# Optimization experiments

Hardware: AMD Instinct MI355X
Metric: run time of the kernel (lower is better)

## Reference

```python
import jax, jax.numpy as jnp
import numpy as np

B, D, C, T = 2048, 512, 128, 151  # batch, hidden, vocab(NUM_CHAR), TEXT_MAX_LEN


def setup_inputs() -> dict:
    key = jax.random.key(0)
    ks = jax.random.split(key, 8)
    s = 1.0 / np.sqrt(D)
    u = lambda k, shape: jax.random.uniform(k, shape, jnp.float32, -s, s)
    return {
        "feat": jax.random.normal(ks[0], (B, D), jnp.float32),  # resnet pooler_output
        "W_ih": u(ks[1], (3 * D, D)),   # GRU input weights (r,z,n stacked, torch layout)
        "W_hh": u(ks[2], (3 * D, D)),   # GRU hidden weights
        "b_ih": u(ks[3], (3 * D,)),
        "b_hh": u(ks[4], (3 * D,)),
        "W_proj": u(ks[5], (C, D)),     # Linear(512, NUM_CHAR)
        "b_proj": u(ks[6], (C,)),
        "embed": jax.random.normal(ks[7], (C, D), jnp.float32),  # Embedding(NUM_CHAR, 512)
    }


def reference(feat, W_ih, W_hh, b_ih, b_hh, W_proj, b_proj, embed):
    def step(carry, _):
        h, x = carry  # [B,D] each
        gi = x @ W_ih.T + b_ih   # [B,3D]
        gh = h @ W_hh.T + b_hh   # [B,3D]
        i_r, i_z, i_n = jnp.split(gi, 3, axis=1)
        h_r, h_z, h_n = jnp.split(gh, 3, axis=1)
        r = jax.nn.sigmoid(i_r + h_r)
        z = jax.nn.sigmoid(i_z + h_z)
        n = jnp.tanh(i_n + r * h_n)
        h_new = (1.0 - z) * n + z * h
        logits = h_new @ W_proj.T + b_proj          # [B,C]
        probs = jax.nn.softmax(logits, axis=1)
        tok = jnp.argmax(probs, axis=1)             # [B]
        x_new = embed[tok]                          # greedy feedback
        return (h_new, x_new), (logits, tok)

    h0 = feat                                        # hidden init = pooled feature
    x0 = jnp.zeros((feat.shape[0], D), feat.dtype)   # zero start token input
    _, (logits_seq, toks_seq) = jax.lax.scan(step, (h0, x0), None, length=T)
    logits = jnp.transpose(logits_seq, (1, 2, 0))    # [B, NUM_CHAR, T]
    tokens = toks_seq.T                              # [B, T]
    return logits, tokens
```

## Files before the change

kernel.cpp:

```cpp
#include <hip/hip_runtime.h>
#include <math.h>

#define BB 2048
#define DD 512
#define CC 128
#define TT 151
#define G3 1536

typedef __bf16 bf16x8 __attribute__((ext_vector_type(8)));
typedef float f32x4 __attribute__((ext_vector_type(4)));


__global__ void k_transpose_wih(const float* __restrict__ Wih, float* __restrict__ WihT) {
    int idx = blockIdx.x * 256 + threadIdx.x;
    if (idx < G3 * DD) {
        int j = idx / DD, k = idx - j * DD;
        WihT[k * G3 + j] = Wih[idx];
    }
}

__global__ void k_pack_wp_frag(const float* __restrict__ Wproj, __bf16* __restrict__ out) {
    int idx = blockIdx.x * 256 + threadIdx.x;
    if (idx >= 131072) return;
    int j = idx & 7;
    int lane = (idx >> 3) & 63;
    int part = (idx >> 9) & 1;
    int kt = (idx >> 10) & 15;
    int w = idx >> 14;
    int c = w * 16 + (lane & 15);
    int k = kt * 32 + (lane >> 4) * 8 + j;
    float v = Wproj[c * DD + k];
    __bf16 hi = (__bf16)v;
    out[idx] = part ? (__bf16)(v - (float)hi) : hi;
}

__global__ void k_pack_whh_frag(const float* __restrict__ Whh, __bf16* __restrict__ out) {
    int idx = blockIdx.x * 256 + threadIdx.x;
    if (idx >= 786432) return;
    int j8 = idx & 7;
    int lane = (idx >> 3) & 63;
    int rest = idx >> 9;
    int tile = rest % 12;
    int kt = (rest / 12) % 16;
    int w = rest / (12 * 16);
    int g = tile >> 2, tl = tile & 3;
    int colc = lane & 15, quad = lane >> 4;
    int jcol = g * 512 + w * 64 + tl * 16 + colc;
    int k = kt * 32 + quad * 8 + j8;
    float v = Whh[jcol * DD + k];
    __bf16 hi = (__bf16)v;
    __bf16 lo = (__bf16)(v - (float)hi);
    size_t base = ((((size_t)w * 16 + kt) * 12 + tile) * 2) * 512 + lane * 8 + j8;
    out[base] = hi;
    out[base + 512] = lo;
}

__global__ void k_build_E(const float* __restrict__ embed, const float* __restrict__ WihT,
                          const float* __restrict__ b_ih, const float* __restrict__ b_hh,
                          float* __restrict__ E) {
    __shared__ float emb[16][DD];
    const int t = threadIdx.x;
    const int j = blockIdx.x * 256 + t;
    const int c0 = blockIdx.y * 16;
    for (int i = 0; i < 16; i++) {
        int c = c0 + i;
        for (int k = t; k < DD; k += 256)
            emb[i][k] = (c < CC) ? embed[c * DD + k] : 0.0f;
    }
    __syncthreads();
    float acc[16];
#pragma unroll
    for (int i = 0; i < 16; i++) acc[i] = 0.0f;
    for (int k = 0; k < DD; k++) {
        float wv = WihT[k * G3 + j];
#pragma unroll
        for (int i = 0; i < 16; i++) acc[i] = fmaf(emb[i][k], wv, acc[i]);
    }
    float bj = b_ih[j] + (j < 1024 ? b_hh[j] : 0.0f);
    for (int i = 0; i < 16; i++) {
        int c = c0 + i;
        if (c <= CC) E[(size_t)c * G3 + j] = acc[i] + bj;
    }
}


__device__ __forceinline__ float fast_sigmoid(float x) {
    return __builtin_amdgcn_rcpf(1.0f + __expf(-x));
}
__device__ __forceinline__ float fast_tanh(float x) {
    x = fminf(10.0f, fmaxf(-10.0f, x));
    float e = __expf(2.0f * x);
    return (e - 1.0f) * __builtin_amdgcn_rcpf(e + 1.0f);
}

__global__ __launch_bounds__(512, 2) void k_gru(
    const float* __restrict__ feat, const __bf16* __restrict__ Whf,
    const __bf16* __restrict__ Wpf, const float* __restrict__ b_proj,
    const float* __restrict__ b_hh, const float* __restrict__ Ep,
    float* __restrict__ out) {
    __shared__ __align__(16) __bf16 h_hi[16][520];
    __shared__ __align__(16) __bf16 h_lo[16][520];
    __shared__ float lgbuf[16][CC][9];
    __shared__ int tok_s[16];

    float* out_logits = out;
    float* out_tok = out + (size_t)BB * CC * TT;

    const int t = threadIdx.x;
    const int w = t >> 6;
    const int lane = t & 63;
    const int row0 = blockIdx.x * 16;
    const int col = lane & 15;
    const int quad = lane >> 4;
    const int bq = quad * 4;

    float ho[4][4];
#pragma unroll
    for (int tile = 0; tile < 4; tile++) {
        const int d = w * 64 + tile * 16 + col;
#pragma unroll
        for (int rg = 0; rg < 4; rg++) {
            const int b = bq + rg;
            float v = feat[(size_t)(row0 + b) * DD + d];
            ho[tile][rg] = v;
            __bf16 hi = (__bf16)v;
            h_hi[b][d] = hi;
            h_lo[b][d] = (__bf16)(v - (float)hi);
        }
    }
    if (t < 16) tok_s[t] = CC;

    const float bp = b_proj[w * 16 + col];
    float bhn_t[4];
#pragma unroll
    for (int tile = 0; tile < 4; tile++)
        bhn_t[tile] = b_hh[1024 + w * 64 + tile * 16 + col];

    const __bf16* wseq = Whf + (size_t)w * 196608;
    const __bf16* wpseq = Wpf + (size_t)w * 16384;
    __syncthreads();

    for (int step = 0; step < TT; step++) {
        const int sl = step & 7;

        f32x4 acc[12];
#pragma unroll
        for (int i = 0; i < 12; i++) acc[i] = (f32x4)(0.0f);
        for (int kt = 0; kt < 16; kt++) {
            bf16x8 ahi = *(const bf16x8*)&h_hi[col][kt * 32 + quad * 8];
            bf16x8 alo = *(const bf16x8*)&h_lo[col][kt * 32 + quad * 8];
            const __bf16* wk = wseq + kt * 12288;
#pragma unroll
            for (int tile = 0; tile < 12; tile++) {
                bf16x8 bhi = *(const bf16x8*)(wk + tile * 1024 + lane * 8);
                bf16x8 blo = *(const bf16x8*)(wk + tile * 1024 + 512 + lane * 8);
                acc[tile] = __builtin_amdgcn_mfma_f32_16x16x32_bf16(ahi, bhi, acc[tile], 0, 0, 0);
                acc[tile] = __builtin_amdgcn_mfma_f32_16x16x32_bf16(alo, bhi, acc[tile], 0, 0, 0);
                acc[tile] = __builtin_amdgcn_mfma_f32_16x16x32_bf16(ahi, blo, acc[tile], 0, 0, 0);
            }
        }
        __syncthreads();

        {
            int tk[4];
#pragma unroll
            for (int rg = 0; rg < 4; rg++) tk[rg] = tok_s[bq + rg];
#pragma unroll
            for (int tile = 0; tile < 4; tile++) {
                const int d = w * 64 + tile * 16 + col;
#pragma unroll
                for (int rg = 0; rg < 4; rg++) {
                    const int b = bq + rg;
                    const float* Er = Ep + (size_t)tk[rg] * G3 + d;
                    float rr = fast_sigmoid(acc[tile][rg] + Er[0]);
                    float zz = fast_sigmoid(acc[4 + tile][rg] + Er[512]);
                    float nn = fast_tanh(Er[1024] + rr * (acc[8 + tile][rg] + bhn_t[tile]));
                    float hv = (1.0f - zz) * nn + zz * ho[tile][rg];
                    ho[tile][rg] = hv;
                    __bf16 hi = (__bf16)hv;
                    h_hi[b][d] = hi;
                    h_lo[b][d] = (__bf16)(hv - (float)hi);
                }
            }
        }
        __syncthreads();

        {
            f32x4 accp = (f32x4)(0.0f);
            for (int kt = 0; kt < 16; kt++) {
                bf16x8 ahi = *(const bf16x8*)&h_hi[col][kt * 32 + quad * 8];
                bf16x8 alo = *(const bf16x8*)&h_lo[col][kt * 32 + quad * 8];
                const __bf16* pk = wpseq + kt * 1024;
                bf16x8 bhi = *(const bf16x8*)(pk + lane * 8);
                bf16x8 blo = *(const bf16x8*)(pk + 512 + lane * 8);
                accp = __builtin_amdgcn_mfma_f32_16x16x32_bf16(ahi, bhi, accp, 0, 0, 0);
                accp = __builtin_amdgcn_mfma_f32_16x16x32_bf16(alo, bhi, accp, 0, 0, 0);
                accp = __builtin_amdgcn_mfma_f32_16x16x32_bf16(ahi, blo, accp, 0, 0, 0);
            }
#pragma unroll
            for (int rg = 0; rg < 4; rg++)
                lgbuf[bq + rg][w * 16 + col][sl] = accp[rg] + bp;
        }
        __syncthreads();

        {
#pragma unroll
            for (int pass = 0; pass < 2; pass++) {
                const int r = w * 2 + pass;
                float v0 = lgbuf[r][lane][sl];
                float v1 = lgbuf[r][lane + 64][sl];
                float bv; int bi;
                if (v0 >= v1) { bv = v0; bi = lane; } else { bv = v1; bi = lane + 64; }
#pragma unroll
                for (int off = 32; off > 0; off >>= 1) {
                    float ov = __shfl_down(bv, off, 64);
                    int oi = __shfl_down(bi, off, 64);
                    if (ov > bv || (ov == bv && oi < bi)) { bv = ov; bi = oi; }
                }
                if (lane == 0) {
                    tok_s[r] = bi;
                    __builtin_nontemporal_store((float)bi, &out_tok[(size_t)(row0 + r) * TT + step]);
                }
            }
        }
        __syncthreads();

        if ((step & 7) == 7 || step == TT - 1) {
            const int t0 = step & ~7;
            const int cnt = step - t0 + 1;
#pragma unroll
            for (int p = 0; p < 4; p++) {
                const int pair = t + p * 512;
                const int b = pair >> 7, c = pair & (CC - 1);
                float* dst = out_logits + ((size_t)(row0 + b) * CC + c) * TT + t0;
                const float* src = &lgbuf[b][c][0];
                for (int s = 0; s < cnt; s++) __builtin_nontemporal_store(src[s], &dst[s]);
            }
        }
    }
}


extern "C" void kernel_launch(void* const* d_in, const int* in_sizes, int n_in,
                              void* d_out, int out_size, void* d_ws, size_t ws_size,
                              hipStream_t stream) {
    const float* feat   = (const float*)d_in[0];
    const float* W_ih   = (const float*)d_in[1];
    const float* W_hh   = (const float*)d_in[2];
    const float* b_ih   = (const float*)d_in[3];
    const float* b_hh   = (const float*)d_in[4];
    const float* W_proj = (const float*)d_in[5];
    const float* b_proj = (const float*)d_in[6];
    const float* embed  = (const float*)d_in[7];
    float* out = (float*)d_out;

    float* ws = (float*)d_ws;
    float*  WihT = ws;
    float*  E    = ws + 786432;
    __bf16* Wpf  = (__bf16*)(ws + 984576);
    __bf16* Whf  = (__bf16*)(ws + 1050112);

    hipLaunchKernelGGL(k_transpose_wih, dim3(3072), dim3(256), 0, stream, W_ih, WihT);
    hipLaunchKernelGGL(k_pack_wp_frag, dim3(512), dim3(256), 0, stream, W_proj, Wpf);
    hipLaunchKernelGGL(k_pack_whh_frag, dim3(3072), dim3(256), 0, stream, W_hh, Whf);
    hipLaunchKernelGGL(k_build_E, dim3(6, 9), dim3(256), 0, stream, embed, WihT, b_ih, b_hh, E);
    hipLaunchKernelGGL(k_gru, dim3(128), dim3(512), 0, stream,
                       feat, Whf, Wpf, b_proj, b_hh, E, out);
}
```

Before: 5.868 ms.

## Split each batch tile's hidden dimension across two cooperating blocks with flag sync

Each group of 16 batch rows is now handled by two workgroups (256 blocks instead of 128). Each one computes half of the hidden units and half of the projection K-range. Every step, the two partners exchange their hidden halves and partial logits through global memory, using release/acquire flags and a spin-wait. The intent is to use all CUs on the chip for the latency-bound sequential recurrence. The cost is a cross-block handshake and global round-trip each step, and a deadlock risk if the partner blocks are not co-resident.

Measured after the change: 20.76 ms. 3.54x slower.

```diff
diff --git a/kernel.cpp b/kernel.cpp
--- a/kernel.cpp
+++ b/kernel.cpp
@@ -17,21 +17,6 @@
         int j = idx / DD, k = idx - j * DD;
         WihT[k * G3 + j] = Wih[idx];
     }
-}
-
-__global__ void k_pack_wp_frag(const float* __restrict__ Wproj, __bf16* __restrict__ out) {
-    int idx = blockIdx.x * 256 + threadIdx.x;
-    if (idx >= 131072) return;
-    int j = idx & 7;
-    int lane = (idx >> 3) & 63;
-    int part = (idx >> 9) & 1;
-    int kt = (idx >> 10) & 15;
-    int w = idx >> 14;
-    int c = w * 16 + (lane & 15);
-    int k = kt * 32 + (lane >> 4) * 8 + j;
-    float v = Wproj[c * DD + k];
-    __bf16 hi = (__bf16)v;
-    out[idx] = part ? (__bf16)(v - (float)hi) : hi;
 }
 
 __global__ void k_pack_whh_frag(const float* __restrict__ Whh, __bf16* __restrict__ out) {
@@ -40,17 +25,36 @@
     int j8 = idx & 7;
     int lane = (idx >> 3) & 63;
     int rest = idx >> 9;
-    int tile = rest % 12;
-    int kt = (rest / 12) % 16;
-    int w = rest / (12 * 16);
-    int g = tile >> 2, tl = tile & 3;
-    int colc = lane & 15, quad = lane >> 4;
-    int jcol = g * 512 + w * 64 + tl * 16 + colc;
-    int k = kt * 32 + quad * 8 + j8;
+    int tile = rest % 6;
+    int kt = (rest / 6) % 16;
+    int w = (rest / 96) % 8;
+    int s = rest / 768;
+    int g = tile >> 1, tl = tile & 1;
+    int jcol = g * 512 + s * 256 + w * 32 + tl * 16 + (lane & 15);
+    int k = kt * 32 + (lane >> 4) * 8 + j8;
     float v = Whh[jcol * DD + k];
     __bf16 hi = (__bf16)v;
     __bf16 lo = (__bf16)(v - (float)hi);
-    size_t base = ((((size_t)w * 16 + kt) * 12 + tile) * 2) * 512 + lane * 8 + j8;
+    size_t base = (size_t)((((s * 8 + w) * 16 + kt) * 6 + tile) * 2) * 512 + lane * 8 + j8;
+    out[base] = hi;
+    out[base + 512] = lo;
+}
+
+__global__ void k_pack_wp_frag(const float* __restrict__ Wproj, __bf16* __restrict__ out) {
+    int idx = blockIdx.x * 256 + threadIdx.x;
+    if (idx >= 65536) return;
+    int j = idx & 7;
+    int lane = (idx >> 3) & 63;
+    int rest = idx >> 9;
+    int kt = rest % 8;
+    int w = (rest / 8) % 8;
+    int s = rest / 64;
+    int c = w * 16 + (lane & 15);
+    int k = s * 256 + kt * 32 + (lane >> 4) * 8 + j;
+    float v = Wproj[c * DD + k];
+    __bf16 hi = (__bf16)v;
+    __bf16 lo = (__bf16)(v - (float)hi);
+    size_t base = (size_t)(((s * 8 + w) * 8 + kt) * 2) * 512 + lane * 8 + j;
     out[base] = hi;
     out[base + 512] = lo;
 }
@@ -97,10 +101,13 @@
     const float* __restrict__ feat, const __bf16* __restrict__ Whf,
     const __bf16* __restrict__ Wpf, const float* __restrict__ b_proj,
     const float* __restrict__ b_hh, const float* __restrict__ Ep,
+    unsigned int* xh, float* xl, int* flags,
     float* __restrict__ out) {
     __shared__ __align__(16) __bf16 h_hi[16][520];
     __shared__ __align__(16) __bf16 h_lo[16][520];
-    __shared__ float lgbuf[16][CC][9];
+    __shared__ float plg[16][CC];
+    __shared__ float lgbuf[16][64][10];
+    __shared__ float bpj[CC];
     __shared__ int tok_s[16];
 
     float* out_logits = out;
@@ -109,49 +116,60 @@
     const int t = threadIdx.x;
     const int w = t >> 6;
     const int lane = t & 63;
-    const int row0 = blockIdx.x * 16;
     const int col = lane & 15;
     const int quad = lane >> 4;
     const int bq = quad * 4;
 
-    float ho[4][4];
-#pragma unroll
-    for (int tile = 0; tile < 4; tile++) {
-        const int d = w * 64 + tile * 16 + col;
-#pragma unroll
-        for (int rg = 0; rg < 4; rg++) {
-            const int b = bq + rg;
-            float v = feat[(size_t)(row0 + b) * DD + d];
-            ho[tile][rg] = v;
-            __bf16 hi = (__bf16)v;
-            h_hi[b][d] = hi;
-            h_lo[b][d] = (__bf16)(v - (float)hi);
-        }
-    }
+    const int bid = blockIdx.x;
+    const int grp = bid & 7;
+    const int s = grp >> 2;
+    const int pair = (bid >> 3) * 4 + (grp & 3);
+    const int row0 = pair * 16;
+    const int fl_self = pair * 2 + s;
+
+    for (int i = 0; i < 16; i++) {
+        float v = feat[(size_t)(row0 + i) * DD + t];
+        __bf16 hi = (__bf16)v;
+        h_hi[i][t] = hi;
+        h_lo[i][t] = (__bf16)(v - (float)hi);
+    }
+    float ho[2][4];
+#pragma unroll
+    for (int tl = 0; tl < 2; tl++) {
+        const int d = s * 256 + w * 32 + tl * 16 + col;
+#pragma unroll
+        for (int rg = 0; rg < 4; rg++)
+            ho[tl][rg] = feat[(size_t)(row0 + bq + rg) * DD + d];
+    }
+    if (t < CC) bpj[t] = b_proj[t];
     if (t < 16) tok_s[t] = CC;
 
-    const float bp = b_proj[w * 16 + col];
-    float bhn_t[4];
-#pragma unroll
-    for (int tile = 0; tile < 4; tile++)
-        bhn_t[tile] = b_hh[1024 + w * 64 + tile * 16 + col];
-
-    const __bf16* wseq = Whf + (size_t)w * 196608;
-    const __bf16* wpseq = Wpf + (size_t)w * 16384;
+    float bhn_t[2];
+#pragma unroll
+    for (int tl = 0; tl < 2; tl++)
+        bhn_t[tl] = b_hh[1024 + s * 256 + w * 32 + tl * 16 + col];
+
+    const __bf16* wseq = Whf + (size_t)(s * 8 + w) * 98304;
+    const __bf16* wpseq = Wpf + (size_t)(s * 8 + w) * 8192;
     __syncthreads();
 
     for (int step = 0; step < TT; step++) {
         const int sl = step & 7;
-
-        f32x4 acc[12];
-#pragma unroll
-        for (int i = 0; i < 12; i++) acc[i] = (f32x4)(0.0f);
+        const int par = step & 1;
+        unsigned int* xh_self = xh + ((size_t)(pair * 2 + par) * 2 + s) * 4096;
+        unsigned int* xh_part = xh + ((size_t)(pair * 2 + par) * 2 + (1 - s)) * 4096;
+        float* xl_self = xl + ((size_t)(pair * 2 + par) * 2 + s) * 2048;
+        float* xl_part = xl + ((size_t)(pair * 2 + par) * 2 + (1 - s)) * 2048;
+
+        f32x4 acc[6];
+#pragma unroll
+        for (int i = 0; i < 6; i++) acc[i] = (f32x4)(0.0f);
         for (int kt = 0; kt < 16; kt++) {
             bf16x8 ahi = *(const bf16x8*)&h_hi[col][kt * 32 + quad * 8];
             bf16x8 alo = *(const bf16x8*)&h_lo[col][kt * 32 + quad * 8];
-            const __bf16* wk = wseq + kt * 12288;
-#pragma unroll
-            for (int tile = 0; tile < 12; tile++) {
+            const __bf16* wk = wseq + kt * 6144;
+#pragma unroll
+            for (int tile = 0; tile < 6; tile++) {
                 bf16x8 bhi = *(const bf16x8*)(wk + tile * 1024 + lane * 8);
                 bf16x8 blo = *(const bf16x8*)(wk + tile * 1024 + 512 + lane * 8);
                 acc[tile] = __builtin_amdgcn_mfma_f32_16x16x32_bf16(ahi, bhi, acc[tile], 0, 0, 0);
@@ -166,20 +184,26 @@
 #pragma unroll
             for (int rg = 0; rg < 4; rg++) tk[rg] = tok_s[bq + rg];
 #pragma unroll
-            for (int tile = 0; tile < 4; tile++) {
-                const int d = w * 64 + tile * 16 + col;
+            for (int tl = 0; tl < 2; tl++) {
+                const int d = s * 256 + w * 32 + tl * 16 + col;
+                const int dl = d - s * 256;
 #pragma unroll
                 for (int rg = 0; rg < 4; rg++) {
                     const int b = bq + rg;
                     const float* Er = Ep + (size_t)tk[rg] * G3 + d;
-                    float rr = fast_sigmoid(acc[tile][rg] + Er[0]);
-                    float zz = fast_sigmoid(acc[4 + tile][rg] + Er[512]);
-                    float nn = fast_tanh(Er[1024] + rr * (acc[8 + tile][rg] + bhn_t[tile]));
-                    float hv = (1.0f - zz) * nn + zz * ho[tile][rg];
-                    ho[tile][rg] = hv;
+                    float rr = fast_sigmoid(acc[tl][rg] + Er[0]);
+                    float zz = fast_sigmoid(acc[2 + tl][rg] + Er[512]);
+                    float nn = fast_tanh(Er[1024] + rr * (acc[4 + tl][rg] + bhn_t[tl]));
+                    float hv = (1.0f - zz) * nn + zz * ho[tl][rg];
+                    ho[tl][rg] = hv;
                     __bf16 hi = (__bf16)hv;
+                    __bf16 lo = (__bf16)(hv - (float)hi);
                     h_hi[b][d] = hi;
-                    h_lo[b][d] = (__bf16)(hv - (float)hi);
+                    h_lo[b][d] = lo;
+                    unsigned int val = ((unsigned int)__builtin_bit_cast(unsigned short, hi) << 16) |
+                                       (unsigned int)__builtin_bit_cast(unsigned short, lo);
+                    __hip_atomic_store(&xh_self[b * 256 + dl], val, __ATOMIC_RELAXED,
+                                       __HIP_MEMORY_SCOPE_AGENT);
                 }
             }
         }
@@ -187,19 +211,55 @@
 
         {
             f32x4 accp = (f32x4)(0.0f);
-            for (int kt = 0; kt < 16; kt++) {
+            for (int ktl = 0; ktl < 8; ktl++) {
+                const int kt = s * 8 + ktl;
                 bf16x8 ahi = *(const bf16x8*)&h_hi[col][kt * 32 + quad * 8];
                 bf16x8 alo = *(const bf16x8*)&h_lo[col][kt * 32 + quad * 8];
-                const __bf16* pk = wpseq + kt * 1024;
+                const __bf16* pk = wpseq + ktl * 1024;
                 bf16x8 bhi = *(const bf16x8*)(pk + lane * 8);
                 bf16x8 blo = *(const bf16x8*)(pk + 512 + lane * 8);
                 accp = __builtin_amdgcn_mfma_f32_16x16x32_bf16(ahi, bhi, accp, 0, 0, 0);
                 accp = __builtin_amdgcn_mfma_f32_16x16x32_bf16(alo, bhi, accp, 0, 0, 0);
                 accp = __builtin_amdgcn_mfma_f32_16x16x32_bf16(ahi, blo, accp, 0, 0, 0);
             }
-#pragma unroll
-            for (int rg = 0; rg < 4; rg++)
-                lgbuf[bq + rg][w * 16 + col][sl] = accp[rg] + bp;
+            const int c = w * 16 + col;
+#pragma unroll
+            for (int rg = 0; rg < 4; rg++) {
+                plg[bq + rg][c] = accp[rg];
+                __hip_atomic_store(&xl_self[(bq + rg) * CC + c], accp[rg], __ATOMIC_RELAXED,
+                                   __HIP_MEMORY_SCOPE_AGENT);
+            }
+        }
+        __syncthreads();
+
+        if (t == 0) {
+            __hip_atomic_store(&flags[fl_self], step + 1, __ATOMIC_RELEASE,
+                               __HIP_MEMORY_SCOPE_AGENT);
+            while (__hip_atomic_load(&flags[fl_self ^ 1], __ATOMIC_ACQUIRE,
+                                     __HIP_MEMORY_SCOPE_AGENT) < step + 1)
+                __builtin_amdgcn_s_sleep(1);
+        }
+        __syncthreads();
+
+        for (int i = 0; i < 8; i++) {
+            const int idx = t + i * 512;
+            const int b = idx >> 8, dl = idx & 255;
+            unsigned int v = __hip_atomic_load(&xh_part[idx], __ATOMIC_RELAXED,
+                                               __HIP_MEMORY_SCOPE_AGENT);
+            h_hi[b][(1 - s) * 256 + dl] = __builtin_bit_cast(__bf16, (unsigned short)(v >> 16));
+            h_lo[b][(1 - s) * 256 + dl] = __builtin_bit_cast(__bf16, (unsigned short)(v & 0xffff));
+        }
+        for (int i = 0; i < 4; i++) {
+            const int idx = t + i * 512;
+            const int b = idx >> 7, c = idx & (CC - 1);
+            float oth = __hip_atomic_load(&xl_part[idx], __ATOMIC_RELAXED,
+                                          __HIP_MEMORY_SCOPE_AGENT);
+            float own = plg[b][c];
+            float p0 = (s == 0) ? own : oth;
+            float p1 = (s == 0) ? oth : own;
+            float lg = (p0 + p1) + bpj[c];
+            plg[b][c] = lg;
+            if ((c >> 6) == s) lgbuf[b][c & 63][sl] = lg;
         }
         __syncthreads();
 
@@ -207,8 +267,8 @@
 #pragma unroll
             for (int pass = 0; pass < 2; pass++) {
                 const int r = w * 2 + pass;
-                float v0 = lgbuf[r][lane][sl];
-                float v1 = lgbuf[r][lane + 64][sl];
+                float v0 = plg[r][lane];
+                float v1 = plg[r][lane + 64];
                 float bv; int bi;
                 if (v0 >= v1) { bv = v0; bi = lane; } else { bv = v1; bi = lane + 64; }
 #pragma unroll
@@ -219,7 +279,9 @@
                 }
                 if (lane == 0) {
                     tok_s[r] = bi;
-                    __builtin_nontemporal_store((float)bi, &out_tok[(size_t)(row0 + r) * TT + step]);
+                    if (s == 0)
+                        __builtin_nontemporal_store(
+                            (float)bi, &out_tok[(size_t)(row0 + r) * TT + step]);
                 }
             }
         }
@@ -229,12 +291,12 @@
             const int t0 = step & ~7;
             const int cnt = step - t0 + 1;
 #pragma unroll
-            for (int p = 0; p < 4; p++) {
-                const int pair = t + p * 512;
-                const int b = pair >> 7, c = pair & (CC - 1);
-                float* dst = out_logits + ((size_t)(row0 + b) * CC + c) * TT + t0;
-                const float* src = &lgbuf[b][c][0];
-                for (int s = 0; s < cnt; s++) __builtin_nontemporal_store(src[s], &dst[s]);
+            for (int p = 0; p < 2; p++) {
+                const int pr = t + p * 512;
+                const int b = pr >> 6, c64 = pr & 63;
+                float* dst = out_logits + ((size_t)(row0 + b) * CC + (s * 64 + c64)) * TT + t0;
+                const float* src = &lgbuf[b][c64][0];
+                for (int q = 0; q < cnt; q++) __builtin_nontemporal_store(src[q], &dst[q]);
             }
         }
     }
@@ -255,15 +317,19 @@
     float* out = (float*)d_out;
 
     float* ws = (float*)d_ws;
-    float*  WihT = ws;
-    float*  E    = ws + 786432;
-    __bf16* Wpf  = (__bf16*)(ws + 984576);
-    __bf16* Whf  = (__bf16*)(ws + 1050112);
-
+    float*        WihT  = ws;
+    float*        E     = ws + 786432;
+    __bf16*       Whf   = (__bf16*)(ws + 984576);
+    __bf16*       Wpf   = (__bf16*)(ws + 1771008);
+    unsigned int* xh    = (unsigned int*)(ws + 1836544);
+    float*        xl    = ws + 3933696;
+    int*          flags = (int*)(ws + 4982272);
+
+    hipMemsetAsync(flags, 0, 256 * sizeof(int), stream);
     hipLaunchKernelGGL(k_transpose_wih, dim3(3072), dim3(256), 0, stream, W_ih, WihT);
-    hipLaunchKernelGGL(k_pack_wp_frag, dim3(512), dim3(256), 0, stream, W_proj, Wpf);
+    hipLaunchKernelGGL(k_pack_wp_frag, dim3(256), dim3(256), 0, stream, W_proj, Wpf);
     hipLaunchKernelGGL(k_pack_whh_frag, dim3(3072), dim3(256), 0, stream, W_hh, Whf);
     hipLaunchKernelGGL(k_build_E, dim3(6, 9), dim3(256), 0, stream, embed, WihT, b_ih, b_hh, E);
-    hipLaunchKernelGGL(k_gru, dim3(128), dim3(512), 0, stream,
-                       feat, Whf, Wpf, b_proj, b_hh, E, out);
-}
+    hipLaunchKernelGGL(k_gru, dim3(256), dim3(512), 0, stream,
+                       feat, Whf, Wpf, b_proj, b_hh, E, xh, xl, flags, out);
+}
```
